# Optimization experiments

Measured on AMD Instinct MI355X. Metric: run time of the kernel, lower is better.

The kernel has to match this reference:

```python
import jax, jax.numpy as jnp
import numpy as np

N_NODES = 50000
N_RELS = 100000
N_TRIPLES = 100000
D = 512          # node_dim == rel_dim
H = 768          # hidden_dim
NUM_LAYERS = 3
B = 16           # number of images (segments)
EPS = 1e-5


def setup_inputs() -> dict:
    key = jax.random.key(0)
    ks = jax.random.split(key, 12)
    node_feats = jax.random.normal(ks[0], (N_NODES, D), dtype=jnp.float32)
    rel_feats = jax.random.normal(ks[1], (N_RELS, D), dtype=jnp.float32)
    subj = jax.random.randint(ks[2], (N_TRIPLES,), 0, N_NODES)
    rel = jax.random.randint(ks[3], (N_TRIPLES,), 0, N_RELS)
    obj = jax.random.randint(ks[4], (N_TRIPLES,), 0, N_NODES)
    triples = jnp.stack([subj, rel, obj], axis=1).astype(jnp.int64)
    obj_to_img = jnp.sort(jax.random.randint(ks[5], (N_NODES,), 0, B))
    obj_to_img = obj_to_img.at[-1].set(B - 1)  # pin batch_size = B (torch uses max+1)
    obj_to_img = obj_to_img.astype(jnp.int64)
    s = 0.02
    params = dict(
        node_in_w=jax.random.normal(ks[6], (H, D), dtype=jnp.float32) * s,
        node_in_b=jnp.zeros((H,), dtype=jnp.float32),
        rel_in_w=jax.random.normal(ks[7], (H, D), dtype=jnp.float32) * s,
        rel_in_b=jnp.zeros((H,), dtype=jnp.float32),
        proj_w=jax.random.normal(ks[8], (NUM_LAYERS, H, 2 * H), dtype=jnp.float32) * s,
        proj_b=jnp.zeros((NUM_LAYERS, H), dtype=jnp.float32),
        ln_node_g=jnp.ones((H,), dtype=jnp.float32),
        ln_node_b=jnp.zeros((H,), dtype=jnp.float32),
        ln_rel_g=jnp.ones((H,), dtype=jnp.float32),
        ln_rel_b=jnp.zeros((H,), dtype=jnp.float32),
    )
    return dict(node_feats=node_feats, rel_feats=rel_feats, triples=triples,
                obj_to_img=obj_to_img, **params)


def _layer_norm(x, g, b):
    mu = jnp.mean(x, axis=-1, keepdims=True)
    var = jnp.var(x, axis=-1, keepdims=True)
    return (x - mu) * jax.lax.rsqrt(var + EPS) * g + b


def reference(node_feats, rel_feats, triples, obj_to_img,
              node_in_w, node_in_b, rel_in_w, rel_in_b,
              proj_w, proj_b, ln_node_g, ln_node_b, ln_rel_g, ln_rel_b):
    subj_idx, rel_idx, obj_idx = triples[:, 0], triples[:, 1], triples[:, 2]

    node_states = node_feats @ node_in_w.T + node_in_b          # (N_nodes, H)
    rel_states = rel_feats @ rel_in_w.T + rel_in_b               # (N_rels, H)

    for l in range(NUM_LAYERS):
        rel_g = rel_states[rel_idx]                              # (T, H)
        msg_s2o = node_states[subj_idx] + rel_g                  # subject -> object
        msg_o2s = node_states[obj_idx] + rel_g                   # object -> subject
        agg = (jax.ops.segment_sum(msg_s2o, obj_idx, num_segments=N_NODES)
               + jax.ops.segment_sum(msg_o2s, subj_idx, num_segments=N_NODES))
        h = jnp.concatenate([node_states, agg], axis=-1)         # (N_nodes, 2H)
        h = h @ proj_w[l].T + proj_b[l]
        h = jax.nn.silu(h)
        node_states = node_states + h                            # residual (dropout=0)

    node_states = _layer_norm(node_states, ln_node_g, ln_node_b)
    rel_states = _layer_norm(rel_states, ln_rel_g, ln_rel_b)

    sums = jax.ops.segment_sum(node_states, obj_to_img, num_segments=B)
    counts = jax.ops.segment_sum(jnp.ones((N_NODES,), node_states.dtype),
                                 obj_to_img, num_segments=B)
    global_states = sums / jnp.clip(counts, 1.0)[:, None]        # (B, H)
    return node_states, global_states
```

## Files before the change

kernel.cpp:

```cpp
#include <hip/hip_runtime.h>
#include <hip/hip_bf16.h>
#include <math.h>

#define N_NODES   50000
#define N_RELS    100000
#define N_TRIPLES 100000
#define D_IN      512
#define H_DIM     768
#define NUM_LAYERS 3
#define B_IMG     16
#define MP        50176

typedef __attribute__((ext_vector_type(8))) short short8;
typedef __attribute__((ext_vector_type(4))) float f32x4;

typedef const __attribute__((address_space(1))) unsigned int glb_u32;
typedef __attribute__((address_space(3))) unsigned int lds_u32;

__device__ inline short f2bf16s(float f){
  union { __hip_bfloat16 h; unsigned short u; } cv;
  cv.h = __float2bfloat16(f);
  return (short)cv.u;
}
__device__ inline float bf2f(unsigned short u){
  union { unsigned u; float f; } c; c.u = ((unsigned)u)<<16; return c.f;
}
__device__ inline uint2 pack4bf(float4 v){
  uint2 r;
  r.x = ((unsigned)(unsigned short)f2bf16s(v.x)) | (((unsigned)(unsigned short)f2bf16s(v.y))<<16);
  r.y = ((unsigned)(unsigned short)f2bf16s(v.z)) | (((unsigned)(unsigned short)f2bf16s(v.w))<<16);
  return r;
}
__device__ inline float4 unpack4bf(uint2 p){
  float4 v;
  v.x = bf2f((unsigned short)(p.x & 0xffff)); v.y = bf2f((unsigned short)(p.x >> 16));
  v.z = bf2f((unsigned short)(p.y & 0xffff)); v.w = bf2f((unsigned short)(p.y >> 16));
  return v;
}

__global__ void detect_idx64_kernel(const unsigned* __restrict__ tr, int* __restrict__ flag){
  if (threadIdx.x == 0 && blockIdx.x == 0){
    unsigned o = 0;
    for (int k = 0; k < 256; k++) o |= tr[2*k + 1];
    flag[0] = (o == 0) ? 1 : 0;
  }
}

__device__ inline void load_triple(const void* tp, int t, int is64, int& s, int& r, int& o){
  if (is64){
    const long long* p = (const long long*)tp;
    s = (int)p[3*t]; r = (int)p[3*t+1]; o = (int)p[3*t+2];
  } else {
    const int* p = (const int*)tp;
    s = p[3*t]; r = p[3*t+1]; o = p[3*t+2];
  }
  s = (s < 0) ? 0 : (s >= N_NODES ? N_NODES-1 : s);
  o = (o < 0) ? 0 : (o >= N_NODES ? N_NODES-1 : o);
  r = (r < 0) ? 0 : (r >= N_RELS  ? N_RELS-1  : r);
}

__device__ inline int idx_at(const void* p, int i, int is64){
  return is64 ? (int)((const long long*)p)[i] : ((const int*)p)[i];
}

__global__ __launch_bounds__(256)
void hist_kernel(const void* __restrict__ tr, const int* __restrict__ flag,
                 int* __restrict__ deg){
  int t = blockIdx.x*256 + threadIdx.x;
  if (t >= N_TRIPLES) return;
  int s, r, o;
  load_triple(tr, t, flag[0], s, r, o);
  atomicAdd(&deg[o], 1);
  atomicAdd(&deg[s], 1);
}

__global__ __launch_bounds__(1024)
void scan_kernel(const int* __restrict__ deg, int* __restrict__ offs,
                 int* __restrict__ cursor, float* __restrict__ cnt){
  __shared__ int partial[1024];
  int tid = threadIdx.x;
  const int per = (N_NODES + 1023)/1024;
  int start = tid*per, end = start+per; if (end > N_NODES) end = N_NODES;
  if (start > N_NODES) start = N_NODES;
  int s = 0;
  for (int i=start; i<end; i++) s += deg[i];
  partial[tid] = s;
  __syncthreads();
  for (int off=1; off<1024; off<<=1){
    int v = (tid >= off) ? partial[tid-off] : 0;
    __syncthreads();
    partial[tid] += v;
    __syncthreads();
  }
  int run = (tid > 0) ? partial[tid-1] : 0;
  for (int i=start; i<end; i++){
    offs[i] = run; cursor[i] = run; cnt[i] = (float)deg[i];
    run += deg[i];
  }
  if (tid == 1023) offs[N_NODES] = run;
}

__global__ __launch_bounds__(256)
void fill_kernel(const void* __restrict__ tr, const int* __restrict__ flag,
                 int* __restrict__ cursor, int* __restrict__ col_node,
                 int* __restrict__ col_rel){
  int t = blockIdx.x*256 + threadIdx.x;
  if (t >= N_TRIPLES) return;
  int s, r, o;
  load_triple(tr, t, flag[0], s, r, o);
  int p1 = atomicAdd(&cursor[o], 1); col_node[p1] = s; col_rel[p1] = r;
  int p2 = atomicAdd(&cursor[s], 1); col_node[p2] = o; col_rel[p2] = r;
}

__global__ __launch_bounds__(256)
void gather_rel_bf_kernel(const int* __restrict__ offs, const int* __restrict__ col_rel,
                          const unsigned short* __restrict__ relf_bf,
                          unsigned short* __restrict__ rfa_bf){
  int v = blockIdx.x*4 + (threadIdx.x >> 6);
  int lane = threadIdx.x & 63;
  float4 a0 = {0,0,0,0}, a1 = {0,0,0,0};
  int lo = offs[v], hi = offs[v+1];
  for (int e=lo; e<hi; e++){
    int r = col_rel[e];
    const uint2* rp = (const uint2*)(relf_bf + (size_t)r*D_IN);
    float4 x0 = unpack4bf(rp[lane]);
    float4 x1 = unpack4bf(rp[lane+64]);
    a0.x+=x0.x; a0.y+=x0.y; a0.z+=x0.z; a0.w+=x0.w;
    a1.x+=x1.x; a1.y+=x1.y; a1.z+=x1.z; a1.w+=x1.w;
  }
  uint2* out = (uint2*)(rfa_bf + (size_t)v*D_IN);
  out[lane]    = pack4bf(a0);
  out[lane+64] = pack4bf(a1);
}

__global__ __launch_bounds__(256)
void gather_rel_kernel(const int* __restrict__ offs, const int* __restrict__ col_rel,
                       const float* __restrict__ relf, unsigned short* __restrict__ rfa_bf){
  int v = blockIdx.x*4 + (threadIdx.x >> 6);
  int lane = threadIdx.x & 63;
  float4 a0 = {0,0,0,0}, a1 = {0,0,0,0};
  int lo = offs[v], hi = offs[v+1];
  for (int e=lo; e<hi; e++){
    int r = col_rel[e];
    const float* rp = relf + (size_t)r*D_IN + lane*4;
    float4 x0 = *(const float4*)rp;
    float4 x1 = *(const float4*)(rp + 256);
    a0.x+=x0.x; a0.y+=x0.y; a0.z+=x0.z; a0.w+=x0.w;
    a1.x+=x1.x; a1.y+=x1.y; a1.z+=x1.z; a1.w+=x1.w;
  }
  uint2* out = (uint2*)(rfa_bf + (size_t)v*D_IN);
  out[lane]    = pack4bf(a0);
  out[lane+64] = pack4bf(a1);
}

__global__ __launch_bounds__(256)
void gather_node_bf_kernel(const int* __restrict__ offs, const int* __restrict__ col_node,
                           const unsigned short* __restrict__ seed_bf,
                           const unsigned short* __restrict__ node_bf,
                           unsigned short* __restrict__ agg_bf){
  int v = blockIdx.x*4 + (threadIdx.x >> 6);
  int lane = threadIdx.x & 63;
  const uint2* sp = (const uint2*)(seed_bf + (size_t)v*H_DIM);
  float4 a0 = unpack4bf(sp[lane]);
  float4 a1 = unpack4bf(sp[lane+64]);
  float4 a2 = unpack4bf(sp[lane+128]);
  int lo = offs[v], hi = offs[v+1];
  for (int e=lo; e<hi; e++){
    int u = col_node[e];
    const uint2* np = (const uint2*)(node_bf + (size_t)u*H_DIM);
    float4 x0 = unpack4bf(np[lane]);
    float4 x1 = unpack4bf(np[lane+64]);
    float4 x2 = unpack4bf(np[lane+128]);
    a0.x+=x0.x; a0.y+=x0.y; a0.z+=x0.z; a0.w+=x0.w;
    a1.x+=x1.x; a1.y+=x1.y; a1.z+=x1.z; a1.w+=x1.w;
    a2.x+=x2.x; a2.y+=x2.y; a2.z+=x2.z; a2.w+=x2.w;
  }
  uint2* out = (uint2*)(agg_bf + (size_t)v*H_DIM);
  out[lane]     = pack4bf(a0);
  out[lane+64]  = pack4bf(a1);
  out[lane+128] = pack4bf(a2);
}

__global__ __launch_bounds__(256)
void gather_node_kernel(const int* __restrict__ offs, const int* __restrict__ col_node,
                        const unsigned short* __restrict__ seed_bf,
                        const float* __restrict__ node,
                        unsigned short* __restrict__ agg_bf){
  int v = blockIdx.x*4 + (threadIdx.x >> 6);
  int lane = threadIdx.x & 63;
  const uint2* sp = (const uint2*)(seed_bf + (size_t)v*H_DIM);
  float4 a0 = unpack4bf(sp[lane]);
  float4 a1 = unpack4bf(sp[lane+64]);
  float4 a2 = unpack4bf(sp[lane+128]);
  int lo = offs[v], hi = offs[v+1];
  for (int e=lo; e<hi; e++){
    int u = col_node[e];
    const float* np = node + (size_t)u*H_DIM + lane*4;
    float4 x0 = *(const float4*)np;
    float4 x1 = *(const float4*)(np + 256);
    float4 x2 = *(const float4*)(np + 512);
    a0.x+=x0.x; a0.y+=x0.y; a0.z+=x0.z; a0.w+=x0.w;
    a1.x+=x1.x; a1.y+=x1.y; a1.z+=x1.z; a1.w+=x1.w;
    a2.x+=x2.x; a2.y+=x2.y; a2.z+=x2.z; a2.w+=x2.w;
  }
  uint2* out = (uint2*)(agg_bf + (size_t)v*H_DIM);
  out[lane]     = pack4bf(a0);
  out[lane+64]  = pack4bf(a1);
  out[lane+128] = pack4bf(a2);
}

__device__ inline short8 load_cvt8(const float* __restrict__ p, bool valid){
  short8 r;
  if (valid){
    float4 v0 = *(const float4*)(p);
    float4 v1 = *(const float4*)(p+4);
    r[0]=f2bf16s(v0.x); r[1]=f2bf16s(v0.y); r[2]=f2bf16s(v0.z); r[3]=f2bf16s(v0.w);
    r[4]=f2bf16s(v1.x); r[5]=f2bf16s(v1.y); r[6]=f2bf16s(v1.z); r[7]=f2bf16s(v1.w);
  } else {
    r = (short8)0;
  }
  return r;
}

template<int MODE>
__global__ __launch_bounds__(512)
void gemm_lds(const unsigned short* __restrict__ A1,
              const unsigned short* __restrict__ A2,
              const unsigned short* __restrict__ W,
              const float* __restrict__ bias,
              const float* __restrict__ rowscale,
              unsigned short* __restrict__ Cbf,
              int M, int K1, int K2)
{
  __shared__ unsigned short As[256*64];
  __shared__ unsigned short Bs[128*64];
  const int lane = threadIdx.x & 63;
  const int wv   = threadIdx.x >> 6;
  const int llo  = lane & 15, lhi = lane >> 4;
  const int wm   = (wv>>1)*64;
  const int wn   = (wv&1)*64;

  const int nwg  = gridDim.x;
  const int q8   = nwg >> 3, r8 = nwg & 7;
  const int xcd  = blockIdx.x & 7, base = blockIdx.x >> 3;
  const int virt = (xcd < r8 ? xcd*(q8+1) : r8*(q8+1) + (xcd-r8)*q8) + base;
  const int bm   = (virt / 6) * 256;
  const int bn   = (virt % 6) * 128;
  const int KW   = K1 + K2;

  const int srow = lane >> 3;
  const int scol = ((lane & 7) ^ srow) * 8;

  f32x4 acc[4][4];
  #pragma unroll
  for (int i=0;i<4;i++)
    #pragma unroll
    for (int j=0;j<4;j++) acc[i][j] = (f32x4)(0.0f);

  const unsigned short* Wb = W + (size_t)bn*KW;

  for (int k0=0; k0<KW; k0+=64){
    const unsigned short* Asrc; int ak0, astr;
    if (k0 < K1){ Asrc = A1 + (size_t)bm*K1; ak0 = k0;      astr = K1; }
    else        { Asrc = A2 + (size_t)bm*K2; ak0 = k0 - K1; astr = K2; }
    #pragma unroll
    for (int p=0;p<4;p++){
      int c = wv*4 + p;
      int row = c*8 + srow;
      __builtin_amdgcn_global_load_lds(
        (glb_u32*)(Asrc + (size_t)row*astr + ak0 + scol),
        (lds_u32*)(As + c*512), 16, 0, 0);
    }
    #pragma unroll
    for (int p=0;p<2;p++){
      int c = wv*2 + p;
      int row = c*8 + srow;
      __builtin_amdgcn_global_load_lds(
        (glb_u32*)(Wb + (size_t)row*KW + k0 + scol),
        (lds_u32*)(Bs + c*512), 16, 0, 0);
    }
    __syncthreads();
    #pragma unroll
    for (int kk=0; kk<64; kk+=32){
      short8 a[4], b[4];
      #pragma unroll
      for (int i=0;i<4;i++){
        int rowA = wm + i*16 + llo;
        int rowB = wn + i*16 + llo;
        int c16  = lhi + (kk>>3);
        a[i] = *(const short8*)(As + rowA*64 + ((c16 ^ (rowA&7))*8));
        b[i] = *(const short8*)(Bs + rowB*64 + ((c16 ^ (rowB&7))*8));
      }
      #pragma unroll
      for (int i=0;i<4;i++)
        #pragma unroll
        for (int j=0;j<4;j++)
          acc[i][j] = __builtin_amdgcn_mfma_f32_16x16x32_bf16(a[i], b[j], acc[i][j], 0,0,0);
    }
    __syncthreads();
  }

  #pragma unroll
  for (int j=0;j<4;j++){
    int col = bn + wn + j*16 + llo;
    float bv = bias ? bias[col] : 0.0f;
    #pragma unroll
    for (int i=0;i<4;i++){
      #pragma unroll
      for (int r=0;r<4;r++){
        int row = bm + wm + i*16 + lhi*4 + r;
        if (row < M){
          size_t idx = (size_t)row*H_DIM + col;
          float v = acc[i][j][r];
          if (MODE==0){
            Cbf[idx] = (unsigned short)f2bf16s(v + bv);
          } else if (MODE==2){
            v += rowscale[row]*bv;
            Cbf[idx] = (unsigned short)f2bf16s(v);
          } else {
            v += bv;
            float s = v / (1.0f + __expf(-v));
            float nv = bf2f(A1[idx]) + s;
            Cbf[idx] = (unsigned short)f2bf16s(nv);
          }
        }
      }
    }
  }
}

template<int MODE, int ABF>
__global__ __launch_bounds__(256)
void gemm_in(const float* __restrict__ Xf, const unsigned short* __restrict__ Xbf,
             const unsigned short* __restrict__ W,
             const float* __restrict__ bias, const float* __restrict__ rowscale,
             float* __restrict__ Cf, unsigned short* __restrict__ Cbf,
             int M, int Ka)
{
  const int lane = threadIdx.x & 63;
  const int wv   = threadIdx.x >> 6;
  const int llo  = lane & 15, lhi = lane >> 4;
  const int bm   = blockIdx.x*128 + (wv>>1)*64;
  const int bn   = blockIdx.y*128 + (wv&1)*64;

  f32x4 acc[4][4];
  #pragma unroll
  for (int i=0;i<4;i++)
    #pragma unroll
    for (int j=0;j<4;j++) acc[i][j] = (f32x4)(0.0f);

  for (int k0=0;k0<Ka;k0+=32){
    short8 a[4], b[4];
    #pragma unroll
    for (int i=0;i<4;i++){
      int row = bm + i*16 + llo;
      if (ABF) a[i] = (row < M) ? *(const short8*)(Xbf + (size_t)row*Ka + k0 + lhi*8) : (short8)0;
      else     a[i] = load_cvt8(Xf + (size_t)row*Ka + k0 + lhi*8, row < M);
      b[i] = *(const short8*)(W + (size_t)(bn + i*16 + llo)*Ka + k0 + lhi*8);
    }
    #pragma unroll
    for (int i=0;i<4;i++)
      #pragma unroll
      for (int j=0;j<4;j++)
        acc[i][j] = __builtin_amdgcn_mfma_f32_16x16x32_bf16(a[i], b[j], acc[i][j], 0,0,0);
  }

  #pragma unroll
  for (int j=0;j<4;j++){
    int col = bn + j*16 + llo;
    float bv = bias ? bias[col] : 0.0f;
    #pragma unroll
    for (int i=0;i<4;i++){
      #pragma unroll
      for (int r=0;r<4;r++){
        int row = bm + i*16 + lhi*4 + r;
        if (row < M){
          size_t idx = (size_t)row*H_DIM + col;
          float v = acc[i][j][r];
          if (MODE==2){
            v += rowscale[row]*bv;
            Cbf[idx] = (unsigned short)f2bf16s(v);
          } else {
            Cf[idx] = v + bv;
          }
        }
      }
    }
  }
}

__global__ __launch_bounds__(512)
void gemm_layer(float* __restrict__ node,
                const unsigned short* __restrict__ agg_bf,
                const unsigned short* __restrict__ W,
                const float* __restrict__ bias,
                int M)
{
  const int lane = threadIdx.x & 63;
  const int wv   = threadIdx.x >> 6;
  const int llo  = lane & 15, lhi = lane >> 4;
  const int bm   = blockIdx.x*64;
  const int bn   = wv*96;

  f32x4 acc[4][6];
  #pragma unroll
  for (int i=0;i<4;i++)
    #pragma unroll
    for (int j=0;j<6;j++) acc[i][j] = (f32x4)(0.0f);

  for (int k0=0;k0<H_DIM;k0+=32){
    short8 a[4], b[6];
    #pragma unroll
    for (int i=0;i<4;i++){
      int row = bm + i*16 + llo;
      a[i] = load_cvt8(node + (size_t)row*H_DIM + k0 + lhi*8, row < M);
    }
    #pragma unroll
    for (int j=0;j<6;j++)
      b[j] = *(const short8*)(W + (size_t)(bn + j*16 + llo)*(2*H_DIM) + k0 + lhi*8);
    #pragma unroll
    for (int i=0;i<4;i++)
      #pragma unroll
      for (int j=0;j<6;j++)
        acc[i][j] = __builtin_amdgcn_mfma_f32_16x16x32_bf16(a[i], b[j], acc[i][j], 0,0,0);
  }
  for (int k0=0;k0<H_DIM;k0+=32){
    short8 a[4], b[6];
    #pragma unroll
    for (int i=0;i<4;i++){
      int row = bm + i*16 + llo;
      a[i] = (row < M) ? *(const short8*)(agg_bf + (size_t)row*H_DIM + k0 + lhi*8) : (short8)0;
    }
    #pragma unroll
    for (int j=0;j<6;j++)
      b[j] = *(const short8*)(W + (size_t)(bn + j*16 + llo)*(2*H_DIM) + H_DIM + k0 + lhi*8);
    #pragma unroll
    for (int i=0;i<4;i++)
      #pragma unroll
      for (int j=0;j<6;j++)
        acc[i][j] = __builtin_amdgcn_mfma_f32_16x16x32_bf16(a[i], b[j], acc[i][j], 0,0,0);
  }

  __syncthreads();

  #pragma unroll
  for (int j=0;j<6;j++){
    int col = bn + j*16 + llo;
    float bv = bias[col];
    #pragma unroll
    for (int i=0;i<4;i++){
      #pragma unroll
      for (int r=0;r<4;r++){
        int row = bm + i*16 + lhi*4 + r;
        if (row < M){
          size_t idx = (size_t)row*H_DIM + col;
          float v = acc[i][j][r] + bv;
          float s = v / (1.0f + __expf(-v));
          node[idx] += s;
        }
      }
    }
  }
}

__global__ __launch_bounds__(256)
void cast_bf16_kernel(const float* __restrict__ src, unsigned short* __restrict__ dst,
                      long n){
  long i = ((long)blockIdx.x*blockDim.x + threadIdx.x)*8;
  long stride = (long)gridDim.x*blockDim.x*8;
  for (; i < n; i += stride){
    float4 v0 = *(const float4*)(src+i);
    float4 v1 = *(const float4*)(src+i+4);
    short8 o;
    o[0]=f2bf16s(v0.x); o[1]=f2bf16s(v0.y); o[2]=f2bf16s(v0.z); o[3]=f2bf16s(v0.w);
    o[4]=f2bf16s(v1.x); o[5]=f2bf16s(v1.y); o[6]=f2bf16s(v1.z); o[7]=f2bf16s(v1.w);
    *(short8*)(dst+i) = o;
  }
}

__global__ __launch_bounds__(256)
void ln_kernel(const float* __restrict__ x, const float* __restrict__ g,
               const float* __restrict__ b, float* __restrict__ out){
  int row = blockIdx.x;
  int t = threadIdx.x;
  const float* xr = x + (size_t)row*H_DIM;
  float v0 = xr[t], v1 = xr[t+256], v2 = xr[t+512];
  float s  = v0+v1+v2;
  float ss = v0*v0+v1*v1+v2*v2;
  for (int off=32; off>0; off>>=1){
    s  += __shfl_down(s,  off);
    ss += __shfl_down(ss, off);
  }
  __shared__ float rs_[4], rss_[4];
  __shared__ float mu_s, rstd_s;
  int lane = t & 63, wv = t >> 6;
  if (lane==0){ rs_[wv]=s; rss_[wv]=ss; }
  __syncthreads();
  if (t==0){
    float S  = rs_[0]+rs_[1]+rs_[2]+rs_[3];
    float SS = rss_[0]+rss_[1]+rss_[2]+rss_[3];
    float mu = S * (1.0f/768.0f);
    float var = SS * (1.0f/768.0f) - mu*mu;
    mu_s = mu; rstd_s = rsqrtf(var + 1e-5f);
  }
  __syncthreads();
  float mu = mu_s, rstd = rstd_s;
  float* orow = out + (size_t)row*H_DIM;
  orow[t]     = (v0-mu)*rstd*g[t]     + b[t];
  orow[t+256] = (v1-mu)*rstd*g[t+256] + b[t+256];
  orow[t+512] = (v2-mu)*rstd*g[t+512] + b[t+512];
}

__global__ __launch_bounds__(256)
void ln_bf_kernel(const unsigned short* __restrict__ xbf, const float* __restrict__ g,
                  const float* __restrict__ b, float* __restrict__ out){
  int row = blockIdx.x;
  int t = threadIdx.x;
  const unsigned short* xr = xbf + (size_t)row*H_DIM;
  float v0 = bf2f(xr[t]), v1 = bf2f(xr[t+256]), v2 = bf2f(xr[t+512]);
  float s  = v0+v1+v2;
  float ss = v0*v0+v1*v1+v2*v2;
  for (int off=32; off>0; off>>=1){
    s  += __shfl_down(s,  off);
    ss += __shfl_down(ss, off);
  }
  __shared__ float rs_[4], rss_[4];
  __shared__ float mu_s, rstd_s;
  int lane = t & 63, wv = t >> 6;
  if (lane==0){ rs_[wv]=s; rss_[wv]=ss; }
  __syncthreads();
  if (t==0){
    float S  = rs_[0]+rs_[1]+rs_[2]+rs_[3];
    float SS = rss_[0]+rss_[1]+rss_[2]+rss_[3];
    float mu = S * (1.0f/768.0f);
    float var = SS * (1.0f/768.0f) - mu*mu;
    mu_s = mu; rstd_s = rsqrtf(var + 1e-5f);
  }
  __syncthreads();
  float mu = mu_s, rstd = rstd_s;
  float* orow = out + (size_t)row*H_DIM;
  orow[t]     = (v0-mu)*rstd*g[t]     + b[t];
  orow[t+256] = (v1-mu)*rstd*g[t+256] + b[t+256];
  orow[t+512] = (v2-mu)*rstd*g[t+512] + b[t+512];
}

__global__ __launch_bounds__(256)
void pool1_kernel(const float* __restrict__ ln, const void* __restrict__ o2i,
                  const int* __restrict__ flag, float* __restrict__ acc){
  const int ROWS = 125;
  int is64 = flag[0];
  int r0 = blockIdx.x*ROWS;
  int t = threadIdx.x;
  float a0=0.f, a1=0.f, a2=0.f;
  int cur = idx_at(o2i, r0, is64);
  cur = (cur < 0) ? 0 : (cur >= B_IMG ? B_IMG-1 : cur);
  for (int r=r0; r<r0+ROWS; r++){
    int img = idx_at(o2i, r, is64);
    img = (img < 0) ? 0 : (img >= B_IMG ? B_IMG-1 : img);
    if (img != cur){
      atomicAdd(&acc[cur*H_DIM + t],       a0);
      atomicAdd(&acc[cur*H_DIM + t + 256], a1);
      atomicAdd(&acc[cur*H_DIM + t + 512], a2);
      a0 = a1 = a2 = 0.f;
      cur = img;
    }
    const float* xr = ln + (size_t)r*H_DIM;
    a0 += xr[t]; a1 += xr[t+256]; a2 += xr[t+512];
  }
  atomicAdd(&acc[cur*H_DIM + t],       a0);
  atomicAdd(&acc[cur*H_DIM + t + 256], a1);
  atomicAdd(&acc[cur*H_DIM + t + 512], a2);
}

__device__ inline int lbound_idx(const void* a, int n, int v, int is64){
  int lo=0, hi=n;
  while (lo<hi){ int m=(lo+hi)>>1; if (idx_at(a,m,is64) < v) lo=m+1; else hi=m; }
  return lo;
}

__global__ __launch_bounds__(256)
void pool2_kernel(const float* __restrict__ acc, const void* __restrict__ o2i,
                  const int* __restrict__ flag, float* __restrict__ gout){
  int is64 = flag[0];
  int img = blockIdx.x;
  int t = threadIdx.x;
  int lo = lbound_idx(o2i, N_NODES, img,   is64);
  int hi = lbound_idx(o2i, N_NODES, img+1, is64);
  float c = (float)(hi-lo);
  if (c < 1.0f) c = 1.0f;
  float inv = 1.0f / c;
  gout[(size_t)img*H_DIM + t]       = acc[img*H_DIM + t]       * inv;
  gout[(size_t)img*H_DIM + t + 256] = acc[img*H_DIM + t + 256] * inv;
  gout[(size_t)img*H_DIM + t + 512] = acc[img*H_DIM + t + 512] * inv;
}

extern "C" void kernel_launch(void* const* d_in, const int* in_sizes, int n_in,
                              void* d_out, int out_size, void* d_ws, size_t ws_size,
                              hipStream_t stream){
  const float* node_feats = (const float*)d_in[0];
  const float* rel_feats  = (const float*)d_in[1];
  const void*  triples    = d_in[2];
  const void*  o2i        = d_in[3];
  const float* node_in_w  = (const float*)d_in[4];
  const float* node_in_b  = (const float*)d_in[5];
  const float* rel_in_w   = (const float*)d_in[6];
  const float* rel_in_b   = (const float*)d_in[7];
  const float* proj_w     = (const float*)d_in[8];
  const float* proj_b     = (const float*)d_in[9];
  const float* ln_g       = (const float*)d_in[10];
  const float* ln_b       = (const float*)d_in[11];

  float* out_nodes  = (float*)d_out;
  float* out_global = (float*)d_out + (size_t)N_NODES*H_DIM;

  const int  tri_blocks = (N_TRIPLES + 255)/256;
  const int  gat_blocks = N_NODES/4;

  size_t off = 0;
  auto alloc = [&](size_t bytes)->void*{
    void* r = (char*)d_ws + off; off += (bytes + 255) & ~(size_t)255; return r;
  };
  unsigned short* w_node     = (unsigned short*)alloc((size_t)H_DIM*D_IN*2);
  unsigned short* w_rel      = (unsigned short*)alloc((size_t)H_DIM*D_IN*2);
  unsigned short* w_proj     = (unsigned short*)alloc((size_t)NUM_LAYERS*H_DIM*2*H_DIM*2);
  unsigned short* rel_agg_bf = (unsigned short*)alloc((size_t)MP*H_DIM*2);
  unsigned short* relf_bf    = (unsigned short*)alloc((size_t)N_RELS*D_IN*2);
  unsigned short* shr_bf     = (unsigned short*)alloc((size_t)MP*D_IN*2);
  unsigned short* node_bf0   = (unsigned short*)alloc((size_t)MP*H_DIM*2);
  unsigned short* node_bf1   = (unsigned short*)alloc((size_t)MP*H_DIM*2);
  unsigned short* agg_bf     = (unsigned short*)alloc((size_t)MP*H_DIM*2);
  float*          cnt        = (float*)alloc((size_t)N_NODES*4);
  int*            deg        = (int*)alloc((size_t)N_NODES*4);
  int*            offs       = (int*)alloc((size_t)(N_NODES+1)*4);
  int*            cursor     = (int*)alloc((size_t)N_NODES*4);
  int*            col_node   = (int*)alloc((size_t)2*N_TRIPLES*4);
  int*            col_rel    = (int*)alloc((size_t)2*N_TRIPLES*4);
  int*            flag       = (int*)alloc(256);
  float*          pool_acc   = (float*)alloc((size_t)B_IMG*H_DIM*4);
  size_t need_full = off;

  detect_idx64_kernel<<<1,64,0,stream>>>((const unsigned*)triples, flag);
  hipMemsetAsync(deg, 0, (size_t)N_NODES*4, stream);
  hist_kernel<<<tri_blocks,256,0,stream>>>(triples, flag, deg);
  scan_kernel<<<1,1024,0,stream>>>(deg, offs, cursor, cnt);
  fill_kernel<<<tri_blocks,256,0,stream>>>(triples, flag, cursor, col_node, col_rel);
  cast_bf16_kernel<<<512,256,0,stream>>>(node_in_w, w_node, (long)H_DIM*D_IN);
  cast_bf16_kernel<<<512,256,0,stream>>>(rel_in_w,  w_rel,  (long)H_DIM*D_IN);
  cast_bf16_kernel<<<2048,256,0,stream>>>(proj_w, w_proj, (long)NUM_LAYERS*H_DIM*2*H_DIM);

  if (ws_size >= need_full){
    const int gg = (MP/256) * (H_DIM/128);

    cast_bf16_kernel<<<2048,256,0,stream>>>(node_feats, shr_bf, (long)N_NODES*D_IN);
    gemm_lds<0><<<gg,512,0,stream>>>(shr_bf, nullptr, w_node, node_in_b, nullptr,
                                     node_bf0, N_NODES, D_IN, 0);

    cast_bf16_kernel<<<2048,256,0,stream>>>(rel_feats, relf_bf, (long)N_RELS*D_IN);
    gather_rel_bf_kernel<<<gat_blocks,256,0,stream>>>(offs, col_rel, relf_bf, shr_bf);
    gemm_lds<2><<<gg,512,0,stream>>>(shr_bf, nullptr, w_rel, rel_in_b, cnt,
                                     rel_agg_bf, N_NODES, D_IN, 0);

    unsigned short* cur = node_bf0;
    unsigned short* nxt = node_bf1;
    for (int l=0; l<NUM_LAYERS; ++l){
      gather_node_bf_kernel<<<gat_blocks,256,0,stream>>>(offs, col_node, rel_agg_bf,
                                                         cur, agg_bf);
      gemm_lds<1><<<gg,512,0,stream>>>(cur, agg_bf,
                                       w_proj + (size_t)l*H_DIM*2*H_DIM,
                                       proj_b + (size_t)l*H_DIM, nullptr,
                                       nxt, N_NODES, H_DIM, H_DIM);
      unsigned short* t = cur; cur = nxt; nxt = t;
    }

    ln_bf_kernel<<<N_NODES,256,0,stream>>>(cur, ln_g, ln_b, out_nodes);
    hipMemsetAsync(pool_acc, 0, (size_t)B_IMG*H_DIM*4, stream);
    pool1_kernel<<<400,256,0,stream>>>(out_nodes, o2i, flag, pool_acc);
    pool2_kernel<<<B_IMG,256,0,stream>>>(pool_acc, o2i, flag, out_global);
  } else {
    size_t off2 = 0;
    auto alloc2 = [&](size_t bytes)->void*{
      void* r = (char*)d_ws + off2; off2 += (bytes + 255) & ~(size_t)255; return r;
    };
    unsigned short* w_node2  = (unsigned short*)alloc2((size_t)H_DIM*D_IN*2);
    unsigned short* w_rel2   = (unsigned short*)alloc2((size_t)H_DIM*D_IN*2);
    unsigned short* w_proj2  = (unsigned short*)alloc2((size_t)NUM_LAYERS*H_DIM*2*H_DIM*2);
    unsigned short* relagg2  = (unsigned short*)alloc2((size_t)N_NODES*H_DIM*2);
    unsigned short* rfa2     = (unsigned short*)alloc2((size_t)N_NODES*D_IN*2);
    unsigned short* agg2     = (unsigned short*)alloc2((size_t)N_NODES*H_DIM*2);
    float* cnt2   = (float*)alloc2((size_t)N_NODES*4);
    int*   deg2   = (int*)alloc2((size_t)N_NODES*4);
    int*   offs2  = (int*)alloc2((size_t)(N_NODES+1)*4);
    int*   cur2   = (int*)alloc2((size_t)N_NODES*4);
    int*   coln2  = (int*)alloc2((size_t)2*N_TRIPLES*4);
    int*   colr2  = (int*)alloc2((size_t)2*N_TRIPLES*4);
    int*   flag2  = (int*)alloc2(256);
    float* pacc2  = (float*)alloc2((size_t)B_IMG*H_DIM*4);
    if (ws_size < off2) return;

    detect_idx64_kernel<<<1,64,0,stream>>>((const unsigned*)triples, flag2);
    hipMemsetAsync(deg2, 0, (size_t)N_NODES*4, stream);
    hist_kernel<<<tri_blocks,256,0,stream>>>(triples, flag2, deg2);
    scan_kernel<<<1,1024,0,stream>>>(deg2, offs2, cur2, cnt2);
    fill_kernel<<<tri_blocks,256,0,stream>>>(triples, flag2, cur2, coln2, colr2);
    cast_bf16_kernel<<<512,256,0,stream>>>(node_in_w, w_node2, (long)H_DIM*D_IN);
    cast_bf16_kernel<<<512,256,0,stream>>>(rel_in_w,  w_rel2,  (long)H_DIM*D_IN);
    cast_bf16_kernel<<<2048,256,0,stream>>>(proj_w, w_proj2, (long)NUM_LAYERS*H_DIM*2*H_DIM);

    const dim3 gemm_grid((N_NODES + 127)/128, H_DIM/128);
    gemm_in<0,0><<<gemm_grid,256,0,stream>>>(node_feats, nullptr, w_node2, node_in_b, nullptr,
                                             out_nodes, nullptr, N_NODES, D_IN);
    gather_rel_kernel<<<gat_blocks,256,0,stream>>>(offs2, colr2, rel_feats, rfa2);
    gemm_in<2,1><<<gemm_grid,256,0,stream>>>(nullptr, rfa2, w_rel2, rel_in_b, cnt2,
                                             nullptr, relagg2, N_NODES, D_IN);
    for (int l=0; l<NUM_LAYERS; ++l){
      gather_node_kernel<<<gat_blocks,256,0,stream>>>(offs2, coln2, relagg2,
                                                      out_nodes, agg2);
      gemm_layer<<<(N_NODES+63)/64,512,0,stream>>>(out_nodes, agg2,
                                                   w_proj2 + (size_t)l*H_DIM*2*H_DIM,
                                                   proj_b + (size_t)l*H_DIM, N_NODES);
    }

    ln_kernel<<<N_NODES,256,0,stream>>>(out_nodes, ln_g, ln_b, out_nodes);
    hipMemsetAsync(pacc2, 0, (size_t)B_IMG*H_DIM*4, stream);
    pool1_kernel<<<400,256,0,stream>>>(out_nodes, o2i, flag2, pacc2);
    pool2_kernel<<<B_IMG,256,0,stream>>>(pacc2, o2i, flag2, out_global);
  }
}
```

Baseline: 1.455 ms.

## Reuse LDS-staged residual in projection GEMM and fuse LayerNorm with pooling

In the MODE 1 projection GEMM, the residual node-state values are captured from the LDS A tile at the k-step whose K range matches the output column tile, so the epilogue no longer reloads them from global memory. Separately, the final LayerNorm and the per-image segment-sum pooling are merged into one kernel of 400 blocks, each handling 125 rows, which removes the re-read of the fp32 normalized output. The trade-off is 32 extra registers per thread in the GEMM, and much less parallelism in the LayerNorm stage (400 blocks running 125 serial rows, each with two barriers, versus one block per row before).

New measurement: 1.635 ms. +12.3%, slower.

```diff
diff --git a/kernel.cpp b/kernel.cpp
--- a/kernel.cpp
+++ b/kernel.cpp
@@ -257,6 +257,8 @@
     #pragma unroll
     for (int j=0;j<4;j++) acc[i][j] = (f32x4)(0.0f);
 
+  unsigned oldp[4][4][2];
+
   const unsigned short* Wb = W + (size_t)bn*KW;
 
   for (int k0=0; k0<KW; k0+=64){
@@ -296,6 +298,23 @@
         #pragma unroll
         for (int j=0;j<4;j++)
           acc[i][j] = __builtin_amdgcn_mfma_f32_16x16x32_bf16(a[i], b[j], acc[i][j], 0,0,0);
+    }
+    if (MODE==1 && k0 == bn + wn){
+      #pragma unroll
+      for (int i=0;i<4;i++)
+        #pragma unroll
+        for (int j=0;j<4;j++)
+          #pragma unroll
+          for (int rp=0;rp<2;rp++){
+            int colk = j*16 + llo;
+            int cidx = (((colk>>3) ^ 0)*0);
+            int row0 = wm + i*16 + lhi*4 + rp*2;
+            int row1 = row0 + 1;
+            unsigned lo16 = As[row0*64 + (((colk>>3) ^ (row0&7))<<3) + (colk&7)];
+            unsigned hi16 = As[row1*64 + (((colk>>3) ^ (row1&7))<<3) + (colk&7)];
+            (void)cidx;
+            oldp[i][j][rp] = lo16 | (hi16<<16);
+          }
     }
     __syncthreads();
   }
@@ -320,7 +339,10 @@
           } else {
             v += bv;
             float s = v / (1.0f + __expf(-v));
-            float nv = bf2f(A1[idx]) + s;
+            unsigned pk = oldp[i][j][r>>1];
+            unsigned short o16 = (r&1) ? (unsigned short)(pk>>16)
+                                       : (unsigned short)(pk & 0xffffu);
+            float nv = bf2f(o16) + s;
             Cbf[idx] = (unsigned short)f2bf16s(nv);
           }
         }
@@ -512,36 +534,63 @@
 }
 
 __global__ __launch_bounds__(256)
-void ln_bf_kernel(const unsigned short* __restrict__ xbf, const float* __restrict__ g,
-                  const float* __restrict__ b, float* __restrict__ out){
-  int row = blockIdx.x;
+void ln_pool_kernel(const unsigned short* __restrict__ xbf, const float* __restrict__ g,
+                    const float* __restrict__ b, const void* __restrict__ o2i,
+                    const int* __restrict__ flag, float* __restrict__ out,
+                    float* __restrict__ acc){
+  const int ROWS = 125;
+  int is64 = flag[0];
+  int r0 = blockIdx.x*ROWS;
   int t = threadIdx.x;
-  const unsigned short* xr = xbf + (size_t)row*H_DIM;
-  float v0 = bf2f(xr[t]), v1 = bf2f(xr[t+256]), v2 = bf2f(xr[t+512]);
-  float s  = v0+v1+v2;
-  float ss = v0*v0+v1*v1+v2*v2;
-  for (int off=32; off>0; off>>=1){
-    s  += __shfl_down(s,  off);
-    ss += __shfl_down(ss, off);
-  }
+  int lane = t & 63, wv = t >> 6;
   __shared__ float rs_[4], rss_[4];
   __shared__ float mu_s, rstd_s;
-  int lane = t & 63, wv = t >> 6;
-  if (lane==0){ rs_[wv]=s; rss_[wv]=ss; }
-  __syncthreads();
-  if (t==0){
-    float S  = rs_[0]+rs_[1]+rs_[2]+rs_[3];
-    float SS = rss_[0]+rss_[1]+rss_[2]+rss_[3];
-    float mu = S * (1.0f/768.0f);
-    float var = SS * (1.0f/768.0f) - mu*mu;
-    mu_s = mu; rstd_s = rsqrtf(var + 1e-5f);
-  }
-  __syncthreads();
-  float mu = mu_s, rstd = rstd_s;
-  float* orow = out + (size_t)row*H_DIM;
-  orow[t]     = (v0-mu)*rstd*g[t]     + b[t];
-  orow[t+256] = (v1-mu)*rstd*g[t+256] + b[t+256];
-  orow[t+512] = (v2-mu)*rstd*g[t+512] + b[t+512];
+  float gg0=g[t], gg1=g[t+256], gg2=g[t+512];
+  float bb0=b[t], bb1=b[t+256], bb2=b[t+512];
+  float a0=0.f, a1=0.f, a2=0.f;
+  int cur = idx_at(o2i, r0, is64);
+  cur = (cur < 0) ? 0 : (cur >= B_IMG ? B_IMG-1 : cur);
+  for (int r=r0; r<r0+ROWS; r++){
+    const unsigned short* xr = xbf + (size_t)r*H_DIM;
+    float v0 = bf2f(xr[t]), v1 = bf2f(xr[t+256]), v2 = bf2f(xr[t+512]);
+    float s  = v0+v1+v2;
+    float ss = v0*v0+v1*v1+v2*v2;
+    for (int off=32; off>0; off>>=1){
+      s  += __shfl_down(s,  off);
+      ss += __shfl_down(ss, off);
+    }
+    if (lane==0){ rs_[wv]=s; rss_[wv]=ss; }
+    __syncthreads();
+    if (t==0){
+      float S  = rs_[0]+rs_[1]+rs_[2]+rs_[3];
+      float SS = rss_[0]+rss_[1]+rss_[2]+rss_[3];
+      float mu = S * (1.0f/768.0f);
+      float var = SS * (1.0f/768.0f) - mu*mu;
+      mu_s = mu; rstd_s = rsqrtf(var + 1e-5f);
+    }
+    __syncthreads();
+    float mu = mu_s, rstd = rstd_s;
+    float o0 = (v0-mu)*rstd*gg0 + bb0;
+    float o1 = (v1-mu)*rstd*gg1 + bb1;
+    float o2 = (v2-mu)*rstd*gg2 + bb2;
+    float* orow = out + (size_t)r*H_DIM;
+    orow[t]     = o0;
+    orow[t+256] = o1;
+    orow[t+512] = o2;
+    int img = idx_at(o2i, r, is64);
+    img = (img < 0) ? 0 : (img >= B_IMG ? B_IMG-1 : img);
+    if (img != cur){
+      atomicAdd(&acc[cur*H_DIM + t],       a0);
+      atomicAdd(&acc[cur*H_DIM + t + 256], a1);
+      atomicAdd(&acc[cur*H_DIM + t + 512], a2);
+      a0 = a1 = a2 = 0.f;
+      cur = img;
+    }
+    a0 += o0; a1 += o1; a2 += o2;
+  }
+  atomicAdd(&acc[cur*H_DIM + t],       a0);
+  atomicAdd(&acc[cur*H_DIM + t + 256], a1);
+  atomicAdd(&acc[cur*H_DIM + t + 512], a2);
 }
 
 __global__ __launch_bounds__(256)
@@ -672,9 +721,8 @@
       unsigned short* t = cur; cur = nxt; nxt = t;
     }
 
-    ln_bf_kernel<<<N_NODES,256,0,stream>>>(cur, ln_g, ln_b, out_nodes);
     hipMemsetAsync(pool_acc, 0, (size_t)B_IMG*H_DIM*4, stream);
-    pool1_kernel<<<400,256,0,stream>>>(out_nodes, o2i, flag, pool_acc);
+    ln_pool_kernel<<<400,256,0,stream>>>(cur, ln_g, ln_b, o2i, flag, out_nodes, pool_acc);
     pool2_kernel<<<B_IMG,256,0,stream>>>(pool_acc, o2i, flag, out_global);
   } else {
     size_t off2 = 0;
```

## Double-buffer LDS tiles in GEMM to overlap global loads with MFMA

Applied to the files above, without the earlier changes.

Splits the GEMM's A and B shared-memory tiles into two buffers. The next K-tile is now loaded straight into LDS while MFMA runs on the current one, and each iteration ends with one explicit waitcnt plus barrier instead of two __syncthreads. The aim is to hide global-to-LDS latency behind compute. In exchange, LDS use doubles to 96KB per block, which may cut occupancy.

Result: slower. 1.674 ms (+15.0%).

```diff
diff --git a/kernel.cpp b/kernel.cpp
--- a/kernel.cpp
+++ b/kernel.cpp
@@ -232,8 +232,8 @@
               unsigned short* __restrict__ Cbf,
               int M, int K1, int K2)
 {
-  __shared__ unsigned short As[256*64];
-  __shared__ unsigned short Bs[128*64];
+  __shared__ unsigned short As[2][256*64];
+  __shared__ unsigned short Bs[2][128*64];
   const int lane = threadIdx.x & 63;
   const int wv   = threadIdx.x >> 6;
   const int llo  = lane & 15, lhi = lane >> 4;
@@ -259,46 +259,63 @@
 
   const unsigned short* Wb = W + (size_t)bn*KW;
 
-  for (int k0=0; k0<KW; k0+=64){
-    const unsigned short* Asrc; int ak0, astr;
-    if (k0 < K1){ Asrc = A1 + (size_t)bm*K1; ak0 = k0;      astr = K1; }
-    else        { Asrc = A2 + (size_t)bm*K2; ak0 = k0 - K1; astr = K2; }
-    #pragma unroll
-    for (int p=0;p<4;p++){
-      int c = wv*4 + p;
-      int row = c*8 + srow;
-      __builtin_amdgcn_global_load_lds(
-        (glb_u32*)(Asrc + (size_t)row*astr + ak0 + scol),
-        (lds_u32*)(As + c*512), 16, 0, 0);
-    }
-    #pragma unroll
-    for (int p=0;p<2;p++){
-      int c = wv*2 + p;
-      int row = c*8 + srow;
-      __builtin_amdgcn_global_load_lds(
-        (glb_u32*)(Wb + (size_t)row*KW + k0 + scol),
-        (lds_u32*)(Bs + c*512), 16, 0, 0);
-    }
-    __syncthreads();
-    #pragma unroll
-    for (int kk=0; kk<64; kk+=32){
-      short8 a[4], b[4];
-      #pragma unroll
-      for (int i=0;i<4;i++){
-        int rowA = wm + i*16 + llo;
-        int rowB = wn + i*16 + llo;
-        int c16  = lhi + (kk>>3);
-        a[i] = *(const short8*)(As + rowA*64 + ((c16 ^ (rowA&7))*8));
-        b[i] = *(const short8*)(Bs + rowB*64 + ((c16 ^ (rowB&7))*8));
-      }
-      #pragma unroll
-      for (int i=0;i<4;i++)
-        #pragma unroll
-        for (int j=0;j<4;j++)
-          acc[i][j] = __builtin_amdgcn_mfma_f32_16x16x32_bf16(a[i], b[j], acc[i][j], 0,0,0);
-    }
-    __syncthreads();
-  }
+#define STAGE(BUF, K0) do{ \
+    int k0_ = (K0); \
+    const unsigned short* Asrc_; int ak0_, astr_; \
+    if (k0_ < K1){ Asrc_ = A1 + (size_t)bm*K1; ak0_ = k0_;      astr_ = K1; } \
+    else         { Asrc_ = A2 + (size_t)bm*K2; ak0_ = k0_ - K1; astr_ = K2; } \
+    unsigned short* asb_ = As[BUF]; \
+    unsigned short* bsb_ = Bs[BUF]; \
+    _Pragma("unroll") \
+    for (int p_=0;p_<4;p_++){ \
+      int c_ = wv*4 + p_; \
+      int row_ = c_*8 + srow; \
+      __builtin_amdgcn_global_load_lds( \
+        (glb_u32*)(Asrc_ + (size_t)row_*astr_ + ak0_ + scol), \
+        (lds_u32*)(asb_ + c_*512), 16, 0, 0); \
+    } \
+    _Pragma("unroll") \
+    for (int p_=0;p_<2;p_++){ \
+      int c_ = wv*2 + p_; \
+      int row_ = c_*8 + srow; \
+      __builtin_amdgcn_global_load_lds( \
+        (glb_u32*)(Wb + (size_t)row_*KW + k0_ + scol), \
+        (lds_u32*)(bsb_ + c_*512), 16, 0, 0); \
+    } }while(0)
+
+#define COMPUTE(BUF) do{ \
+    const unsigned short* asb_ = As[BUF]; \
+    const unsigned short* bsb_ = Bs[BUF]; \
+    _Pragma("unroll") \
+    for (int kk=0; kk<64; kk+=32){ \
+      short8 a_[4], b_[4]; \
+      _Pragma("unroll") \
+      for (int i=0;i<4;i++){ \
+        int rowA_ = wm + i*16 + llo; \
+        int rowB_ = wn + i*16 + llo; \
+        int c16_  = lhi + (kk>>3); \
+        a_[i] = *(const short8*)(asb_ + rowA_*64 + ((c16_ ^ (rowA_&7))*8)); \
+        b_[i] = *(const short8*)(bsb_ + rowB_*64 + ((c16_ ^ (rowB_&7))*8)); \
+      } \
+      _Pragma("unroll") \
+      for (int i=0;i<4;i++) \
+        _Pragma("unroll") \
+        for (int j=0;j<4;j++) \
+          acc[i][j] = __builtin_amdgcn_mfma_f32_16x16x32_bf16(a_[i], b_[j], acc[i][j], 0,0,0); \
+    } }while(0)
+
+  const int NT = KW/64;
+  STAGE(0, 0);
+  asm volatile("s_waitcnt vmcnt(0)\ns_barrier" ::: "memory");
+  int cur = 0;
+  for (int t = 0; t < NT; ++t){
+    if (t+1 < NT) STAGE(cur^1, (t+1)*64);
+    COMPUTE(cur);
+    asm volatile("s_waitcnt vmcnt(0)\ns_barrier" ::: "memory");
+    cur ^= 1;
+  }
+#undef STAGE
+#undef COMPUTE
 
   #pragma unroll
   for (int j=0;j<4;j++){
```
